# Kernel tuning notes

Hardware: AMD Instinct MI355X
Metric: run time of the kernel (lower is better)

The kernel has to match this reference:

```python
import jax, jax.numpy as jnp
import numpy as np

K, D, Q, N = 32, 256, 16, 4096
LOG2PI = float(np.log(2.0 * np.pi))


def setup_inputs() -> dict:
    key = jax.random.key(0)
    k1, k2, k3, k4 = jax.random.split(key, 4)
    X = jax.random.normal(k1, (N, D), dtype=jnp.float32)
    log_pi = jnp.full((K,), -np.log(K), dtype=jnp.float32)  # uniform mixture weights
    mu = 0.1 * jax.random.normal(k2, (K, D), dtype=jnp.float32)
    Lambda = 0.1 * jax.random.normal(k3, (K, D, Q), dtype=jnp.float32)
    log_psi = np.float32(np.log(0.01)) + 0.1 * jax.random.normal(k4, (K, D), dtype=jnp.float32)
    return {"X": X, "log_pi": log_pi, "mu": mu, "Lambda": Lambda, "log_psi": log_psi}


def reference(X, log_pi, mu, Lambda, log_psi):
    """MFA e_step: per-component Gaussian log-prob with C_k = L_k L_k^T + diag(psi_k) + jitter.
    Returns (log_resp_norm [N,K], log_likelihood [N]) — same math as the torch loop, batched over K."""
    d = X.shape[1]
    psi = jnp.exp(log_psi) + 1e-6                       # [K,D]
    C = jnp.einsum('kdq,keq->kde', Lambda, Lambda)       # [K,D,D] low-rank part
    C = C + jnp.eye(d, dtype=X.dtype) * (psi + 1e-5)[:, None, :]  # add diag(psi) + 1e-5 jitter
    chol = jnp.linalg.cholesky(C)                        # [K,D,D]
    diff = X[None, :, :] - mu[:, None, :]                # [K,N,D]
    # solve chol @ y = diff^T  (batched lower-triangular solve)
    y = jax.scipy.linalg.solve_triangular(chol, diff.transpose(0, 2, 1), lower=True)  # [K,D,N]
    maha = jnp.sum(y * y, axis=1)                        # [K,N]
    logdet = 2.0 * jnp.sum(jnp.log(jnp.diagonal(chol, axis1=1, axis2=2)), axis=1)  # [K]
    log_prob = -0.5 * (maha + d * LOG2PI + logdet[:, None])  # [K,N]
    log_resps = log_prob.T + log_pi[None, :]             # [N,K]
    log_likelihood = jax.scipy.special.logsumexp(log_resps, axis=1)  # [N]
    log_resp_norm = log_resps - log_likelihood[:, None]
    return log_resp_norm, log_likelihood
```

## Files before the change

kernel.cpp:

```cpp
#include <hip/hip_runtime.h>
#include <math.h>

#define KC 32
#define DD 256
#define QQ 16
#define NPTS 4096
#define NROW 16
#define LOG2PI_F 1.8378770664093453f

typedef unsigned short ushort_t;

#define OFF_U    0
#define OFF_LOGC 512
#define OFF_HB   544

__device__ __forceinline__ ushort_t f2bf(float f) {
    union { float f; unsigned int u; } c; c.f = f;
    unsigned int u = c.u;
    return (ushort_t)((u + 0x7FFFu + ((u >> 16) & 1u)) >> 16);
}
__device__ __forceinline__ float bf2f(ushort_t h) {
    union { unsigned int u; float f; } c; c.u = ((unsigned int)h) << 16;
    return c.f;
}

using short8 = __attribute__((ext_vector_type(8))) short;
using f32x4  = __attribute__((ext_vector_type(4))) float;

#define HSTR 264
__global__ __launch_bounds__(256) void precompute_kernel(
    const float* __restrict__ log_pi, const float* __restrict__ mu,
    const float* __restrict__ Lambda, const float* __restrict__ log_psi,
    float* __restrict__ ws)
{
    __shared__ __align__(16) ushort_t lamH[QQ * HSTR];
    __shared__ __align__(16) ushort_t lhatH[QQ * HSTR];
    __shared__ __align__(16) ushort_t smuH[QQ * HSTR];
    __shared__ float sM[QQ * 17];
    __shared__ float sL[QQ * 17];
    __shared__ float sY[QQ * 17];
    __shared__ float sCol[QQ];
    __shared__ float sPart[8];
    __shared__ float sScal[2];

    const int k = blockIdx.x;
    const int tid = threadIdx.x;
    const int lane = tid & 63;
    const int wave = tid >> 6;
    ushort_t* hb = (ushort_t*)(ws + OFF_HB);
    const int d = tid;

    float Psi  = expf(log_psi[k * DD + d]) + 1.1e-5f;
    float vinv = 1.0f / Psi;
    float mud  = mu[k * DD + d];
    float wv   = vinv * mud;
    hb[(512 + k) * DD + d] = f2bf(vinv);
    hb[(544 + k) * DD + d] = f2bf(wv);
    smuH[d] = f2bf(mud);
    float logPsi = logf(Psi);
    float ckp = wv * mud;

    {
        const float4* lrow = reinterpret_cast<const float4*>(Lambda + (size_t)(k * DD + d) * QQ);
#pragma unroll
        for (int i = 0; i < 4; ++i) {
            float4 t = lrow[i];
            float l0 = t.x, l1 = t.y, l2 = t.z, l3 = t.w;
            int q = 4 * i;
            lamH[(q + 0) * HSTR + d] = f2bf(l0);
            lamH[(q + 1) * HSTR + d] = f2bf(l1);
            lamH[(q + 2) * HSTR + d] = f2bf(l2);
            lamH[(q + 3) * HSTR + d] = f2bf(l3);
            ushort_t h0 = f2bf(l0 * vinv), h1 = f2bf(l1 * vinv);
            ushort_t h2 = f2bf(l2 * vinv), h3 = f2bf(l3 * vinv);
            lhatH[(q + 0) * HSTR + d] = h0;
            lhatH[(q + 1) * HSTR + d] = h1;
            lhatH[(q + 2) * HSTR + d] = h2;
            lhatH[(q + 3) * HSTR + d] = h3;
            hb[(k * QQ + q + 0) * DD + d] = h0;
            hb[(k * QQ + q + 1) * DD + d] = h1;
            hb[(k * QQ + q + 2) * DD + d] = h2;
            hb[(k * QQ + q + 3) * DD + d] = h3;
        }
    }
#pragma unroll
    for (int i = 0; i < 4; ++i) {
        int idx = tid + i * 256;
        if (idx < 990)
            *reinterpret_cast<ushort4*>(smuH + HSTR + idx * 4) = make_ushort4(0, 0, 0, 0);
    }

    float r0 = logPsi, r1 = ckp;
#pragma unroll
    for (int off = 32; off >= 1; off >>= 1) {
        r0 += __shfl_down(r0, off);
        r1 += __shfl_down(r1, off);
    }
    if ((tid & 63) == 0) { sPart[wave] = r0; sPart[4 + wave] = r1; }
    __syncthreads();
    if (tid == 0) {
        sScal[0] = sPart[0] + sPart[1] + sPart[2] + sPart[3];
        sScal[1] = sPart[4] + sPart[5] + sPart[6] + sPart[7];
    }

    if (wave == 0) {
        const int arow = lane & 15;
        const int quad = lane >> 4;
        const ushort_t* pa = lhatH + arow * HSTR + quad * 8;
        const ushort_t* pl = lamH  + arow * HSTR + quad * 8;
        const ushort_t* pm = smuH  + arow * HSTR + quad * 8;
        f32x4 accM = (f32x4){0.f, 0.f, 0.f, 0.f};
        f32x4 accU = (f32x4){0.f, 0.f, 0.f, 0.f};
#pragma unroll
        for (int ks = 0; ks < 8; ++ks) {
            short8 a = *reinterpret_cast<const short8*>(pa + ks * 32);
            accM = __builtin_amdgcn_mfma_f32_16x16x32_bf16(
                a, *reinterpret_cast<const short8*>(pl + ks * 32), accM, 0, 0, 0);
            accU = __builtin_amdgcn_mfma_f32_16x16x32_bf16(
                a, *reinterpret_cast<const short8*>(pm + ks * 32), accU, 0, 0, 0);
        }
#pragma unroll
        for (int reg = 0; reg < 4; ++reg) {
            int q = quad * 4 + reg;
            sM[q * 17 + arow] = accM[reg] + ((q == arow) ? 1.0f : 0.0f);
        }
        if (arow == 0) {
#pragma unroll
            for (int reg = 0; reg < 4; ++reg)
                ws[OFF_U + k * QQ + quad * 4 + reg] = accU[reg];
        }
    }
    __syncthreads();

    if (wave == 0 && lane < QQ) {
        const int r = lane;
        float m[QQ], l[QQ];
#pragma unroll
        for (int c = 0; c < QQ; ++c) m[c] = sM[r * 17 + c];
#pragma unroll
        for (int j = 0; j < QQ; ++j) {
            float djj = __shfl(m[j], j);
            float rinv = 1.0f / sqrtf(djj);
            l[j] = m[j] * rinv;
            sCol[r] = l[j];
#pragma unroll
            for (int c = 0; c < QQ; ++c)
                if (c > j) m[c] -= l[j] * sCol[c];
        }
#pragma unroll
        for (int j = 0; j < QQ; ++j) sL[r * 17 + j] = l[j];
        float dl = logf(l[r]);
        dl += __shfl_xor(dl, 1); dl += __shfl_xor(dl, 2);
        dl += __shfl_xor(dl, 4); dl += __shfl_xor(dl, 8);
        if (r == 0) sPart[1] = dl;
    }
    __syncthreads();

    if (wave == 0 && lane < QQ) {
        const int c = lane;
        float y[QQ];
#pragma unroll
        for (int j = 0; j < QQ; ++j) {
            float acc = (j == c) ? 1.0f : 0.0f;
#pragma unroll
            for (int i = 0; i < QQ; ++i)
                if (i < j) acc -= sL[j * 17 + i] * y[i];
            y[j] = acc / sL[j * 17 + j];
        }
#pragma unroll
        for (int j = 0; j < QQ; ++j) sY[j * 17 + c] = y[j];
    }
    __syncthreads();

    {
        int q = tid >> 4, r = tid & 15;
        float acc = 0.f;
#pragma unroll
        for (int j = 0; j < QQ; ++j) acc += sY[j * 17 + q] * sY[j * 17 + r];
        hb[(576 + k) * DD + tid] = f2bf(acc);
    }
    if (tid == 0) {
        float logdet = sScal[0] + 2.0f * sPart[1];
        ws[OFF_LOGC + k] = log_pi[k] - 0.5f * ((float)DD * LOG2PI_F + logdet)
                         - 0.5f * sScal[1];
    }
}

#define SXH 264
#define TSTR 520
#define QSTR 68
#define SRS 36

__global__ __launch_bounds__(512, 2) void main_kernel(
    const float* __restrict__ X, const float* __restrict__ ws,
    float* __restrict__ out)
{
    const int tid  = threadIdx.x;
    const int lane = tid & 63;
    const int wave = tid >> 6;
    const int n0   = blockIdx.x * NROW;
    const ushort_t* hB = (const ushort_t*)(ws + OFF_HB);

    __shared__ __align__(16) ushort_t xh[NROW * SXH];
    __shared__ __align__(16) ushort_t sT[NROW * TSTR];
    __shared__ __align__(16) float    sQS[NROW * QSTR];
    __shared__ float sU[512];
    __shared__ float sLogc[KC];
    __shared__ float sR[NROW * SRS];
    __shared__ float sLse[NROW];

    {
        const float4* gx = reinterpret_cast<const float4*>(X + (size_t)n0 * DD);
#pragma unroll
        for (int i = 0; i < 2; ++i) {
            int f = tid + i * 512;
            int row = f >> 6, d4 = f & 63;
            float4 v = gx[f];
            *reinterpret_cast<ushort4*>(&xh[row * SXH + d4 * 4]) =
                make_ushort4(f2bf(v.x), f2bf(v.y), f2bf(v.z), f2bf(v.w));
        }
        sU[tid] = ws[OFF_U + tid];
        if (tid < KC) sLogc[tid] = ws[OFF_LOGC + tid];
    }
    __syncthreads();

    {
        const int arow = lane & 15;
        const int quad = lane >> 4;
        short8 a[8];
        const ushort_t* ab = xh + arow * SXH + quad * 8;
#pragma unroll
        for (int ks = 0; ks < 8; ++ks) a[ks] = *reinterpret_cast<const short8*>(ab + ks * 32);

#pragma unroll
        for (int i = 0; i < 4; ++i) {
            const int tile = wave * 4 + i;
            const ushort_t* gB = hB + (size_t)(tile * 16 + arow) * DD + quad * 8;
            f32x4 acc = (f32x4){0.f, 0.f, 0.f, 0.f};
#pragma unroll
            for (int ks = 0; ks < 8; ++ks)
                acc = __builtin_amdgcn_mfma_f32_16x16x32_bf16(
                    a[ks], *reinterpret_cast<const short8*>(gB + ks * 32), acc, 0, 0, 0);
            float uu = sU[tile * 16 + arow];
#pragma unroll
            for (int r = 0; r < 4; ++r)
                sT[(quad * 4 + r) * TSTR + tile * 16 + arow] = f2bf(acc[r] - uu);
        }
        if (wave < 4) {
            short8 aa[8];
            if (wave < 2) {
#pragma unroll
                for (int ks = 0; ks < 8; ++ks) {
                    short8 sq;
#pragma unroll
                    for (int e = 0; e < 8; ++e) {
                        float xf = bf2f((ushort_t)a[ks][e]);
                        sq[e] = (short)f2bf(xf * xf);
                    }
                    aa[ks] = sq;
                }
            } else {
#pragma unroll
                for (int ks = 0; ks < 8; ++ks) aa[ks] = a[ks];
            }
            const ushort_t* gB = hB + (size_t)(512 + wave * 16 + arow) * DD + quad * 8;
            f32x4 acc = (f32x4){0.f, 0.f, 0.f, 0.f};
#pragma unroll
            for (int ks = 0; ks < 8; ++ks)
                acc = __builtin_amdgcn_mfma_f32_16x16x32_bf16(
                    aa[ks], *reinterpret_cast<const short8*>(gB + ks * 32), acc, 0, 0, 0);
            const int col = (wave & 1) * 16 + arow + ((wave >> 1) & 1) * 32;
#pragma unroll
            for (int r = 0; r < 4; ++r)
                sQS[(quad * 4 + r) * QSTR + col] = acc[r];
        }
    }
    __syncthreads();

    {
        const int half = tid & 1;
        const int row  = (tid >> 1) & 15;
        const int c0   = tid >> 5;
#pragma unroll
        for (int ci = 0; ci < 2; ++ci) {
            const int c = c0 + ci * 16;
            float t[16];
            {
                const ushort_t* tp = sT + row * TSTR + c * 16;
                short8 t0 = *reinterpret_cast<const short8*>(tp);
                short8 t1 = *reinterpret_cast<const short8*>(tp + 8);
#pragma unroll
                for (int e = 0; e < 8; ++e) {
                    t[e]     = bf2f((ushort_t)t0[e]);
                    t[8 + e] = bf2f((ushort_t)t1[e]);
                }
            }
            const ushort_t* mp = hB + (size_t)(576 + c) * DD + half * 128;
            float corr = 0.f;
#pragma unroll
            for (int q = 0; q < 8; ++q) {
                short8 m0 = *reinterpret_cast<const short8*>(mp + q * 16);
                short8 m1 = *reinterpret_cast<const short8*>(mp + q * 16 + 8);
                float inner = 0.f;
#pragma unroll
                for (int e = 0; e < 8; ++e)
                    inner += bf2f((ushort_t)m0[e]) * t[e] + bf2f((ushort_t)m1[e]) * t[8 + e];
                corr += t[half * 8 + q] * inner;
            }
            corr += __shfl_xor(corr, 1);
            if (half == 0) {
                float qx = sQS[row * QSTR + c];
                float sx = sQS[row * QSTR + 32 + c];
                sR[row * SRS + c] = sLogc[c] - 0.5f * (qx - 2.0f * sx - corr);
            }
        }
    }
    __syncthreads();

    if (tid < NROW) {
        float m = -INFINITY;
#pragma unroll
        for (int c = 0; c < KC; ++c) m = fmaxf(m, sR[tid * SRS + c]);
        float sum = 0.f;
#pragma unroll
        for (int c = 0; c < KC; ++c) sum += expf(sR[tid * SRS + c] - m);
        float lse = m + logf(sum);
        sLse[tid] = lse;
        out[(size_t)NPTS * KC + n0 + tid] = lse;
    }
    __syncthreads();
    if (tid < NROW * 8) {
        int r = tid >> 3, i = tid & 7;
        float lse = sLse[r];
        float4 v = *reinterpret_cast<const float4*>(sR + r * SRS + i * 4);
        float4 o = make_float4(v.x - lse, v.y - lse, v.z - lse, v.w - lse);
        *reinterpret_cast<float4*>(out + (size_t)(n0 + r) * KC + i * 4) = o;
    }
}

extern "C" void kernel_launch(void* const* d_in, const int* in_sizes, int n_in,
                              void* d_out, int out_size, void* d_ws, size_t ws_size,
                              hipStream_t stream)
{
    (void)in_sizes; (void)n_in; (void)out_size; (void)ws_size;
    const float* X       = (const float*)d_in[0];
    const float* log_pi  = (const float*)d_in[1];
    const float* mu      = (const float*)d_in[2];
    const float* Lambda  = (const float*)d_in[3];
    const float* log_psi = (const float*)d_in[4];
    float* out = (float*)d_out;
    float* ws  = (float*)d_ws;

    precompute_kernel<<<dim3(KC), dim3(256), 0, stream>>>(log_pi, mu, Lambda, log_psi, ws);
    main_kernel<<<dim3(NPTS / NROW), dim3(512), 0, stream>>>(X, ws, out);
}
```

Measured before the change: 84.90 us.

## Stage Minv in LDS, batch B loads before MFMAs, merge precompute Cholesky phases

The main kernel now copies the per-component 16x16 correction matrices into shared memory once per block, so the correction loop reads LDS instead of global memory. It also loads all four B tiles into registers before running the MFMA chain, interleaving four independent accumulators to hide load latency. The precompute kernel merges the Cholesky and triangular-inverse phases into a single wave section, dropping two barriers and reusing padding in sL as the column broadcast buffer. The costs are more LDS per block (about 17KB) and higher register pressure from the 32 short8 B fragments, which could reduce occupancy under launch_bounds(512,2).

```diff
diff --git a/kernel.cpp b/kernel.cpp
--- a/kernel.cpp
+++ b/kernel.cpp
@@ -39,7 +39,6 @@
     __shared__ float sM[QQ * 17];
     __shared__ float sL[QQ * 17];
     __shared__ float sY[QQ * 17];
-    __shared__ float sCol[QQ];
     __shared__ float sPart[8];
     __shared__ float sScal[2];
 
@@ -129,46 +128,41 @@
             for (int reg = 0; reg < 4; ++reg)
                 ws[OFF_U + k * QQ + quad * 4 + reg] = accU[reg];
         }
-    }
-    __syncthreads();
-
-    if (wave == 0 && lane < QQ) {
-        const int r = lane;
-        float m[QQ], l[QQ];
-#pragma unroll
-        for (int c = 0; c < QQ; ++c) m[c] = sM[r * 17 + c];
-#pragma unroll
-        for (int j = 0; j < QQ; ++j) {
-            float djj = __shfl(m[j], j);
-            float rinv = 1.0f / sqrtf(djj);
-            l[j] = m[j] * rinv;
-            sCol[r] = l[j];
-#pragma unroll
-            for (int c = 0; c < QQ; ++c)
-                if (c > j) m[c] -= l[j] * sCol[c];
-        }
-#pragma unroll
-        for (int j = 0; j < QQ; ++j) sL[r * 17 + j] = l[j];
-        float dl = logf(l[r]);
-        dl += __shfl_xor(dl, 1); dl += __shfl_xor(dl, 2);
-        dl += __shfl_xor(dl, 4); dl += __shfl_xor(dl, 8);
-        if (r == 0) sPart[1] = dl;
-    }
-    __syncthreads();
-
-    if (wave == 0 && lane < QQ) {
-        const int c = lane;
-        float y[QQ];
-#pragma unroll
-        for (int j = 0; j < QQ; ++j) {
-            float acc = (j == c) ? 1.0f : 0.0f;
-#pragma unroll
-            for (int i = 0; i < QQ; ++i)
-                if (i < j) acc -= sL[j * 17 + i] * y[i];
-            y[j] = acc / sL[j * 17 + j];
-        }
-#pragma unroll
-        for (int j = 0; j < QQ; ++j) sY[j * 17 + c] = y[j];
+
+        if (lane < QQ) {
+            const int r = lane;
+            float m[QQ], l[QQ];
+#pragma unroll
+            for (int c = 0; c < QQ; ++c) m[c] = sM[r * 17 + c];
+#pragma unroll
+            for (int j = 0; j < QQ; ++j) {
+                float djj = __shfl(m[j], j);
+                float rinv = 1.0f / sqrtf(djj);
+                l[j] = m[j] * rinv;
+                sL[r * 17 + 16] = l[j];
+#pragma unroll
+                for (int c = 0; c < QQ; ++c)
+                    if (c > j) m[c] -= l[j] * sL[c * 17 + 16];
+            }
+#pragma unroll
+            for (int j = 0; j < QQ; ++j) sL[r * 17 + j] = l[j];
+            float dl = logf(l[r]);
+            dl += __shfl_xor(dl, 1); dl += __shfl_xor(dl, 2);
+            dl += __shfl_xor(dl, 4); dl += __shfl_xor(dl, 8);
+            if (r == 0) sPart[1] = dl;
+
+            float y[QQ];
+#pragma unroll
+            for (int j = 0; j < QQ; ++j) {
+                float acc = (j == r) ? 1.0f : 0.0f;
+#pragma unroll
+                for (int i = 0; i < QQ; ++i)
+                    if (i < j) acc -= sL[j * 17 + i] * y[i];
+                y[j] = acc / sL[j * 17 + j];
+            }
+#pragma unroll
+            for (int j = 0; j < QQ; ++j) sY[j * 17 + r] = y[j];
+        }
     }
     __syncthreads();
 
@@ -189,6 +183,7 @@
 #define SXH 264
 #define TSTR 520
 #define QSTR 68
+#define MSTR 264
 #define SRS 36
 
 __global__ __launch_bounds__(512, 2) void main_kernel(
@@ -203,6 +198,7 @@
 
     __shared__ __align__(16) ushort_t xh[NROW * SXH];
     __shared__ __align__(16) ushort_t sT[NROW * TSTR];
+    __shared__ __align__(16) ushort_t sMin[KC * MSTR];
     __shared__ __align__(16) float    sQS[NROW * QSTR];
     __shared__ float sU[512];
     __shared__ float sLogc[KC];
@@ -219,6 +215,13 @@
             *reinterpret_cast<ushort4*>(&xh[row * SXH + d4 * 4]) =
                 make_ushort4(f2bf(v.x), f2bf(v.y), f2bf(v.z), f2bf(v.w));
         }
+#pragma unroll
+        for (int i = 0; i < 4; ++i) {
+            int f = tid + i * 512;
+            int row = f >> 6, c4 = f & 63;
+            *reinterpret_cast<ushort4*>(&sMin[row * MSTR + c4 * 4]) =
+                *reinterpret_cast<const ushort4*>(hB + (size_t)(576 + row) * DD + c4 * 4);
+        }
         sU[tid] = ws[OFF_U + tid];
         if (tid < KC) sLogc[tid] = ws[OFF_LOGC + tid];
     }
@@ -232,19 +235,29 @@
 #pragma unroll
         for (int ks = 0; ks < 8; ++ks) a[ks] = *reinterpret_cast<const short8*>(ab + ks * 32);
 
+        short8 b[4][8];
+#pragma unroll
+        for (int i = 0; i < 4; ++i) {
+            const ushort_t* gB = hB + (size_t)((wave * 4 + i) * 16 + arow) * DD + quad * 8;
+#pragma unroll
+            for (int ks = 0; ks < 8; ++ks)
+                b[i][ks] = *reinterpret_cast<const short8*>(gB + ks * 32);
+        }
+        f32x4 acc[4];
+#pragma unroll
+        for (int i = 0; i < 4; ++i) acc[i] = (f32x4){0.f, 0.f, 0.f, 0.f};
+#pragma unroll
+        for (int ks = 0; ks < 8; ++ks)
+#pragma unroll
+            for (int i = 0; i < 4; ++i)
+                acc[i] = __builtin_amdgcn_mfma_f32_16x16x32_bf16(a[ks], b[i][ks], acc[i], 0, 0, 0);
 #pragma unroll
         for (int i = 0; i < 4; ++i) {
             const int tile = wave * 4 + i;
-            const ushort_t* gB = hB + (size_t)(tile * 16 + arow) * DD + quad * 8;
-            f32x4 acc = (f32x4){0.f, 0.f, 0.f, 0.f};
-#pragma unroll
-            for (int ks = 0; ks < 8; ++ks)
-                acc = __builtin_amdgcn_mfma_f32_16x16x32_bf16(
-                    a[ks], *reinterpret_cast<const short8*>(gB + ks * 32), acc, 0, 0, 0);
             float uu = sU[tile * 16 + arow];
 #pragma unroll
             for (int r = 0; r < 4; ++r)
-                sT[(quad * 4 + r) * TSTR + tile * 16 + arow] = f2bf(acc[r] - uu);
+                sT[(quad * 4 + r) * TSTR + tile * 16 + arow] = f2bf(acc[i][r] - uu);
         }
         if (wave < 4) {
             short8 aa[8];
@@ -264,15 +277,15 @@
                 for (int ks = 0; ks < 8; ++ks) aa[ks] = a[ks];
             }
             const ushort_t* gB = hB + (size_t)(512 + wave * 16 + arow) * DD + quad * 8;
-            f32x4 acc = (f32x4){0.f, 0.f, 0.f, 0.f};
+            f32x4 accs = (f32x4){0.f, 0.f, 0.f, 0.f};
 #pragma unroll
             for (int ks = 0; ks < 8; ++ks)
-                acc = __builtin_amdgcn_mfma_f32_16x16x32_bf16(
-                    aa[ks], *reinterpret_cast<const short8*>(gB + ks * 32), acc, 0, 0, 0);
+                accs = __builtin_amdgcn_mfma_f32_16x16x32_bf16(
+                    aa[ks], *reinterpret_cast<const short8*>(gB + ks * 32), accs, 0, 0, 0);
             const int col = (wave & 1) * 16 + arow + ((wave >> 1) & 1) * 32;
 #pragma unroll
             for (int r = 0; r < 4; ++r)
-                sQS[(quad * 4 + r) * QSTR + col] = acc[r];
+                sQS[(quad * 4 + r) * QSTR + col] = accs[r];
         }
     }
     __syncthreads();
@@ -295,7 +308,7 @@
                     t[8 + e] = bf2f((ushort_t)t1[e]);
                 }
             }
-            const ushort_t* mp = hB + (size_t)(576 + c) * DD + half * 128;
+            const ushort_t* mp = sMin + c * MSTR + half * 128;
             float corr = 0.f;
 #pragma unroll
             for (int q = 0; q < 8; ++q) {
```

Result: no change. 84.27 us (-0.7%).
